# Kernel tuning notes

Hardware: AMD Instinct MI355X
Metric: run time of the kernel (lower is better)

## Reference

```python
import jax, jax.numpy as jnp
import numpy as np

N0, N1, N2 = 100000, 20000, 4000
DEG = 10
G_NODES = 200000
D, ED, CD, FF, NHEAD = 512, 256, 300, 2048, 2


def _layernorm(x, g, b, eps=1e-5):
    m = jnp.mean(x, -1, keepdims=True)
    v = jnp.var(x, -1, keepdims=True)
    return (x - m) * jax.lax.rsqrt(v + eps) * g + b


def _mha(q_in, kv_in, w_in, b_in, w_out, b_out):
    # torch nn.MultiheadAttention, inputs are (seq, batch, d)
    d = q_in.shape[-1]
    wq, wk, wv = w_in[:d], w_in[d:2 * d], w_in[2 * d:]
    bq, bk, bv = b_in[:d], b_in[d:2 * d], b_in[2 * d:]
    dh = d // NHEAD
    q = (q_in @ wq.T + bq).reshape(q_in.shape[0], q_in.shape[1], NHEAD, dh)
    k = (kv_in @ wk.T + bk).reshape(kv_in.shape[0], kv_in.shape[1], NHEAD, dh)
    v = (kv_in @ wv.T + bv).reshape(kv_in.shape[0], kv_in.shape[1], NHEAD, dh)
    scores = jnp.einsum('qnhd,knhd->nhqk', q, k) * (dh ** -0.5)
    o = jnp.einsum('nhqk,knhd->qnhd', jax.nn.softmax(scores, -1), v)
    o = o.reshape(q_in.shape[0], q_in.shape[1], d)
    return o @ w_out.T + b_out


def setup_inputs() -> dict:
    key = jax.random.key(0)
    k = lambda i: jax.random.fold_in(key, i)
    inp = {}
    inp['nid0'] = jax.random.randint(k(0), (N0,), 0, G_NODES, dtype=jnp.int32)
    inp['nid1'] = jax.random.randint(k(1), (N1,), 0, G_NODES, dtype=jnp.int32)
    inp['nid2'] = jax.random.randint(k(2), (N2,), 0, G_NODES, dtype=jnp.int32)
    inp['esrc0'] = jax.random.randint(k(3), (N1 * DEG,), 0, N0, dtype=jnp.int32)
    inp['edst0'] = jnp.repeat(jnp.arange(N1, dtype=jnp.int32), DEG)
    inp['esrc1'] = jax.random.randint(k(4), (N2 * DEG,), 0, N1, dtype=jnp.int32)
    inp['edst1'] = jnp.repeat(jnp.arange(N2, dtype=jnp.int32), DEG)
    inp['content0'] = jax.random.normal(k(5), (N0, CD), jnp.float32)
    inp['content1'] = jax.random.normal(k(6), (N1, CD), jnp.float32)
    inp['content2'] = jax.random.normal(k(7), (N2, CD), jnp.float32)
    inp['node_emb_w'] = jax.random.normal(k(8), (G_NODES + 1, ED), jnp.float32) / ED
    inp['ee_w'] = jax.random.normal(k(9), (D, ED), jnp.float32) * 0.06
    inp['ee_b'] = jax.random.normal(k(10), (D,), jnp.float32) * 0.001
    inp['proj_w'] = jax.random.normal(k(11), (D, CD), jnp.float32) * 0.06
    inp['proj_b'] = jax.random.normal(k(12), (D,), jnp.float32) * 0.001
    inp['proj_g'] = jnp.ones((D,), jnp.float32)
    inp['proj_beta'] = jnp.zeros((D,), jnp.float32)
    L = 2  # decoder layers
    inp['sa_in_w'] = jax.random.normal(k(13), (L, 3 * D, D), jnp.float32) * 0.04
    inp['sa_in_b'] = jnp.zeros((L, 3 * D), jnp.float32)
    inp['sa_out_w'] = jax.random.normal(k(14), (L, D, D), jnp.float32) * 0.04
    inp['sa_out_b'] = jnp.zeros((L, D), jnp.float32)
    inp['ca_in_w'] = jax.random.normal(k(15), (L, 3 * D, D), jnp.float32) * 0.04
    inp['ca_in_b'] = jnp.zeros((L, 3 * D), jnp.float32)
    inp['ca_out_w'] = jax.random.normal(k(16), (L, D, D), jnp.float32) * 0.04
    inp['ca_out_b'] = jnp.zeros((L, D), jnp.float32)
    inp['lin1_w'] = jax.random.normal(k(17), (L, FF, D), jnp.float32) * 0.03
    inp['lin1_b'] = jnp.zeros((L, FF), jnp.float32)
    inp['lin2_w'] = jax.random.normal(k(18), (L, D, FF), jnp.float32) * 0.03
    inp['lin2_b'] = jnp.zeros((L, D), jnp.float32)
    for n in ('n1', 'n2', 'n3'):
        inp[n + '_g'] = jnp.ones((L, D), jnp.float32)
        inp[n + '_b'] = jnp.zeros((L, D), jnp.float32)
    return inp


def _forward(nid0, nid1, nid2, esrc0, edst0, esrc1, edst1,
             content0, content1, content2, node_emb_w, ee_w, ee_b,
             proj_w, proj_b, proj_g, proj_beta,
             sa_in_w, sa_in_b, sa_out_w, sa_out_b,
             ca_in_w, ca_in_b, ca_out_w, ca_out_b,
             lin1_w, lin1_b, lin2_w, lin2_b,
             n1_g, n1_b, n2_g, n2_b, n3_g, n3_b):
    def node_h(nid, content):
        nh = node_emb_w[nid + 1] @ ee_w.T + ee_b           # emb_expand(node_emb(nid+1))
        c = _layernorm(jax.nn.leaky_relu(content @ proj_w.T + proj_b, 0.1), proj_g, proj_beta)
        h = nh + c                                          # mix_embeddings (c[:, :D] == c)
        return h / jnp.maximum(jnp.linalg.norm(h, axis=1, keepdims=True), 1e-5)

    h0 = node_h(nid0, content0)
    h1 = node_h(nid1, content1)
    h2 = node_h(nid2, content2)

    def agg_mean(h_src, src, dst, n_dst):
        s = jax.ops.segment_sum(h_src[src], dst, num_segments=n_dst)
        w = jax.ops.segment_sum(jnp.ones(src.shape[0], h_src.dtype), dst, num_segments=n_dst)
        return s / w[:, None]

    # block 0: non-prediction GraphConv -> concat(mean_agg, h), L2 normalize
    m1 = agg_mean(h0, esrc0, edst0, N1)
    h1 = jnp.concatenate([m1, h1], axis=1)                  # (N1, 2D)
    h1 = h1 / jnp.maximum(jnp.linalg.norm(h1, axis=1, keepdims=True), 1e-5)

    # block 1: prediction GraphConv -> transformer-decoder fusion
    m2 = agg_mean(h1, esrc1, edst1, N2)                     # (N2, 2D)
    mem = m2.reshape(N2, 2, D).transpose(1, 0, 2)           # (n_layer=2, N2, D)
    tgt = h2[None]                                          # (1, N2, D)
    for l in range(2):  # post-norm TransformerDecoderLayer, gelu, dropout=0
        t2 = _mha(tgt, tgt, sa_in_w[l], sa_in_b[l], sa_out_w[l], sa_out_b[l])
        tgt = _layernorm(tgt + t2, n1_g[l], n1_b[l])
        t2 = _mha(tgt, mem, ca_in_w[l], ca_in_b[l], ca_out_w[l], ca_out_b[l])
        tgt = _layernorm(tgt + t2, n2_g[l], n2_b[l])
        ff = jax.nn.gelu(tgt @ lin1_w[l].T + lin1_b[l], approximate=False) @ lin2_w[l].T + lin2_b[l]
        tgt = _layernorm(tgt + ff, n3_g[l], n3_b[l])
    out = tgt[0]                                            # squeeze -> (N2, D)
    return out / jnp.maximum(jnp.linalg.norm(out, axis=1, keepdims=True), 1e-5)


def reference(nid0, nid1, nid2, esrc0, edst0, esrc1, edst1,
              content0, content1, content2, node_emb_w, ee_w, ee_b,
              proj_w, proj_b, proj_g, proj_beta,
              sa_in_w, sa_in_b, sa_out_w, sa_out_b,
              ca_in_w, ca_in_b, ca_out_w, ca_out_b,
              lin1_w, lin1_b, lin2_w, lin2_b,
              n1_g, n1_b, n2_g, n2_b, n3_g, n3_b):
    return _forward(nid0, nid1, nid2, esrc0, edst0, esrc1, edst1,
                    content0, content1, content2, node_emb_w, ee_w, ee_b,
                    proj_w, proj_b, proj_g, proj_beta,
                    sa_in_w, sa_in_b, sa_out_w, sa_out_b,
                    ca_in_w, ca_in_b, ca_out_w, ca_out_b,
                    lin1_w, lin1_b, lin2_w, lin2_b,
                    n1_g, n1_b, n2_g, n2_b, n3_g, n3_b)
```

## Files before the change

### kernel.cpp

```cpp
#include <hip/hip_runtime.h>
#include <math.h>

static constexpr int kN0  = 100000;
static constexpr int kN1  = 20000;
static constexpr int kN2  = 4000;
static constexpr int kDeg = 10;
static constexpr int kD   = 512;
static constexpr int kFF  = 2048;
static constexpr int kRows  = 48;
static constexpr int kRowsN = 32;
static constexpr int kLdA  = 584;
static constexpr int kLdG  = 520;

using short8  = __attribute__((ext_vector_type(8))) short;
using floatx4 = __attribute__((ext_vector_type(4))) float;

__device__ inline unsigned short f2bf(float f) {
    union { float f; unsigned u; } v; v.f = f;
    unsigned r = v.u + 0x7FFFu + ((v.u >> 16) & 1u);
    return (unsigned short)(r >> 16);
}

__global__ __launch_bounds__(256) void pack_node_w_kernel(
    const float* __restrict__ ee_w, const float* __restrict__ proj_w,
    ushort* __restrict__ Bp)
{
    int tid  = blockIdx.x * 256 + threadIdx.x;
    int lane = tid & 63;
    int tile = tid >> 6;
    int n     = (tile & 31) * 16 + (lane & 15);
    int kbase = (tile >> 5) * 32 + (lane >> 4) * 8;
    ushort v[8];
    #pragma unroll
    for (int j = 0; j < 8; ++j) {
        int k = kbase + j;
        float f = 0.f;
        if (k < 256)      f = ee_w[(size_t)n * 256 + k];
        else if (k < 556) f = proj_w[(size_t)n * 300 + (k - 256)];
        v[j] = f2bf(f);
    }
    uint4 u;
    u.x = (unsigned)v[0] | ((unsigned)v[1] << 16);
    u.y = (unsigned)v[2] | ((unsigned)v[3] << 16);
    u.z = (unsigned)v[4] | ((unsigned)v[5] << 16);
    u.w = (unsigned)v[6] | ((unsigned)v[7] << 16);
    *(uint4*)(Bp + (size_t)tid * 8) = u;
}

__global__ __launch_bounds__(256) void pack512_many_kernel(
    const float* __restrict__ sa_in_w, const float* __restrict__ sa_out_w,
    const float* __restrict__ ca_in_w, const float* __restrict__ ca_out_w,
    ushort* __restrict__ dst)
{
    int y = blockIdx.y, l = y / 6, m = y % 6;
    const float* W;
    switch (m) {
        case 0: W = sa_in_w  + (size_t)l * 3 * kD * kD + (size_t)2 * kD * kD; break;
        case 1: W = sa_out_w + (size_t)l * kD * kD; break;
        case 2: W = ca_in_w  + (size_t)l * 3 * kD * kD; break;
        case 3: W = ca_in_w  + (size_t)l * 3 * kD * kD + (size_t)kD * kD; break;
        case 4: W = ca_in_w  + (size_t)l * 3 * kD * kD + (size_t)2 * kD * kD; break;
        default:W = ca_out_w + (size_t)l * kD * kD; break;
    }
    int tid  = blockIdx.x * 256 + threadIdx.x;
    int lane = tid & 63;
    int tile = tid >> 6;
    int n  = (tile & 31) * 16 + (lane & 15);
    int kb = (tile >> 5) * 32 + (lane >> 4) * 8;
    const float* src = W + (size_t)n * 512 + kb;
    ushort v[8];
    #pragma unroll
    for (int j = 0; j < 8; ++j) v[j] = f2bf(src[j]);
    uint4 u;
    u.x = (unsigned)v[0] | ((unsigned)v[1] << 16);
    u.y = (unsigned)v[2] | ((unsigned)v[3] << 16);
    u.z = (unsigned)v[4] | ((unsigned)v[5] << 16);
    u.w = (unsigned)v[6] | ((unsigned)v[7] << 16);
    *(uint4*)(dst + (size_t)y * 262144 + (size_t)tid * 8) = u;
}

__global__ __launch_bounds__(256) void pack_generic_kernel(
    const float* __restrict__ src, size_t srcStride,
    ushort* __restrict__ dst, size_t dstStride, int N, int K)
{
    int tid  = blockIdx.x * 256 + threadIdx.x;
    int NT = N >> 4;
    int lane = tid & 63;
    int tile = tid >> 6;
    int ct = tile % NT, kc = tile / NT;
    int n  = ct * 16 + (lane & 15);
    int kb = kc * 32 + (lane >> 4) * 8;
    const float* W = src + blockIdx.y * srcStride + (size_t)n * K + kb;
    ushort v[8];
    #pragma unroll
    for (int j = 0; j < 8; ++j) v[j] = f2bf(W[j]);
    uint4 u;
    u.x = (unsigned)v[0] | ((unsigned)v[1] << 16);
    u.y = (unsigned)v[2] | ((unsigned)v[3] << 16);
    u.z = (unsigned)v[4] | ((unsigned)v[5] << 16);
    u.w = (unsigned)v[6] | ((unsigned)v[7] << 16);
    *(uint4*)(dst + blockIdx.y * dstStride + (size_t)tid * 8) = u;
}

__global__ __launch_bounds__(512, 4) void node_h_mfma(
    const int* __restrict__ nid,
    const float* __restrict__ content,
    const float* __restrict__ node_emb_w,
    const ushort* __restrict__ Bp,
    const float* __restrict__ ee_b, const float* __restrict__ proj_b,
    const float* __restrict__ proj_g, const float* __restrict__ proj_beta,
    float* __restrict__ hout, int ldh, int n)
{
    __shared__ __align__(16) ushort As[kRowsN * kLdA];
    __shared__ float redS[8][kRowsN], redQ[8][kRowsN];
    __shared__ float meanv[kRowsN], rstdv[kRowsN], rowinv[kRowsN];

    const int t    = threadIdx.x;
    const int lane = t & 63;
    const int wv   = t >> 6;
    const int quad = lane >> 4;
    const int l15  = lane & 15;
    const int row0 = blockIdx.x * kRowsN;

    #pragma unroll
    for (int it = 0; it < 9; ++it) {
        int flat = it * 512 + t;
        int r  = flat / 144;
        int k4 = flat - r * 144;
        int row = row0 + r; if (row >= n) row = n - 1;
        float4 f = make_float4(0.f, 0.f, 0.f, 0.f);
        if (k4 < 64)
            f = *(const float4*)(node_emb_w + ((size_t)(nid[row] + 1)) * 256 + k4 * 4);
        else if (k4 < 139)
            f = *(const float4*)(content + (size_t)row * 300 + (k4 - 64) * 4);
        ushort4 o = make_ushort4(f2bf(f.x), f2bf(f.y), f2bf(f.z), f2bf(f.w));
        *(ushort4*)(As + (size_t)r * kLdA + k4 * 4) = o;
    }
    __syncthreads();

    floatx4 acc[2][4] = {};
    const short8* BpV = (const short8*)Bp;

    #pragma unroll
    for (int kc = 8; kc < 18; ++kc) {
        const short8* bp = BpV + (size_t)(kc * 32 + wv * 4) * 64 + lane;
        short8 b0 = bp[0], b1 = bp[64], b2 = bp[128], b3 = bp[192];
        short8 a[2];
        #pragma unroll
        for (int rt = 0; rt < 2; ++rt)
            a[rt] = *(const short8*)(As + (size_t)(rt * 16 + l15) * kLdA + kc * 32 + quad * 8);
        #pragma unroll
        for (int rt = 0; rt < 2; ++rt) {
            acc[rt][0] = __builtin_amdgcn_mfma_f32_16x16x32_bf16(a[rt], b0, acc[rt][0], 0, 0, 0);
            acc[rt][1] = __builtin_amdgcn_mfma_f32_16x16x32_bf16(a[rt], b1, acc[rt][1], 0, 0, 0);
            acc[rt][2] = __builtin_amdgcn_mfma_f32_16x16x32_bf16(a[rt], b2, acc[rt][2], 0, 0, 0);
            acc[rt][3] = __builtin_amdgcn_mfma_f32_16x16x32_bf16(a[rt], b3, acc[rt][3], 0, 0, 0);
        }
    }

    const int colbase = wv * 64 + l15;
    float pb[4], pg[4], pbt[4], eb[4];
    #pragma unroll
    for (int ct = 0; ct < 4; ++ct) {
        int c = colbase + ct * 16;
        pb[ct]  = proj_b[c];
        pg[ct]  = proj_g[c];
        pbt[ct] = proj_beta[c];
        eb[ct]  = ee_b[c];
    }

    float s8[8], q8[8];
    #pragma unroll
    for (int rt = 0; rt < 2; ++rt) {
        #pragma unroll
        for (int i = 0; i < 4; ++i) {
            float s = 0.f, q = 0.f;
            #pragma unroll
            for (int ct = 0; ct < 4; ++ct) {
                float c = acc[rt][ct][i] + pb[ct];
                c = (c >= 0.f) ? c : 0.1f * c;
                acc[rt][ct][i] = c;
                s += c; q = fmaf(c, c, q);
            }
            s8[rt * 4 + i] = s; q8[rt * 4 + i] = q;
        }
    }
    #pragma unroll
    for (int idx = 0; idx < 8; ++idx) {
        #pragma unroll
        for (int m = 1; m < 16; m <<= 1) {
            s8[idx] += __shfl_xor(s8[idx], m);
            q8[idx] += __shfl_xor(q8[idx], m);
        }
    }
    if (l15 == 0) {
        #pragma unroll
        for (int rt = 0; rt < 2; ++rt)
            #pragma unroll
            for (int i = 0; i < 4; ++i) {
                int rl = rt * 16 + quad * 4 + i;
                redS[wv][rl] = s8[rt * 4 + i];
                redQ[wv][rl] = q8[rt * 4 + i];
            }
    }
    __syncthreads();
    if (t < kRowsN) {
        float s = 0.f, q = 0.f;
        #pragma unroll
        for (int w = 0; w < 8; ++w) { s += redS[w][t]; q += redQ[w][t]; }
        float m   = s * (1.f / 512.f);
        float var = q * (1.f / 512.f) - m * m;
        meanv[t] = m;
        rstdv[t] = rsqrtf(var + 1e-5f);
    }
    __syncthreads();

    #pragma unroll
    for (int rt = 0; rt < 2; ++rt) {
        #pragma unroll
        for (int i = 0; i < 4; ++i) {
            int rl = rt * 16 + quad * 4 + i;
            float m = meanv[rl], rs = rstdv[rl];
            #pragma unroll
            for (int ct = 0; ct < 4; ++ct)
                acc[rt][ct][i] = (acc[rt][ct][i] - m) * rs * pg[ct] + pbt[ct] + eb[ct];
        }
    }

    #pragma unroll
    for (int kc = 0; kc < 8; ++kc) {
        const short8* bp = BpV + (size_t)(kc * 32 + wv * 4) * 64 + lane;
        short8 b0 = bp[0], b1 = bp[64], b2 = bp[128], b3 = bp[192];
        short8 a[2];
        #pragma unroll
        for (int rt = 0; rt < 2; ++rt)
            a[rt] = *(const short8*)(As + (size_t)(rt * 16 + l15) * kLdA + kc * 32 + quad * 8);
        #pragma unroll
        for (int rt = 0; rt < 2; ++rt) {
            acc[rt][0] = __builtin_amdgcn_mfma_f32_16x16x32_bf16(a[rt], b0, acc[rt][0], 0, 0, 0);
            acc[rt][1] = __builtin_amdgcn_mfma_f32_16x16x32_bf16(a[rt], b1, acc[rt][1], 0, 0, 0);
            acc[rt][2] = __builtin_amdgcn_mfma_f32_16x16x32_bf16(a[rt], b2, acc[rt][2], 0, 0, 0);
            acc[rt][3] = __builtin_amdgcn_mfma_f32_16x16x32_bf16(a[rt], b3, acc[rt][3], 0, 0, 0);
        }
    }

    #pragma unroll
    for (int rt = 0; rt < 2; ++rt) {
        #pragma unroll
        for (int i = 0; i < 4; ++i) {
            float psq = 0.f;
            #pragma unroll
            for (int ct = 0; ct < 4; ++ct)
                psq = fmaf(acc[rt][ct][i], acc[rt][ct][i], psq);
            q8[rt * 4 + i] = psq;
        }
    }
    #pragma unroll
    for (int idx = 0; idx < 8; ++idx)
        #pragma unroll
        for (int m = 1; m < 16; m <<= 1)
            q8[idx] += __shfl_xor(q8[idx], m);
    if (l15 == 0) {
        #pragma unroll
        for (int rt = 0; rt < 2; ++rt)
            #pragma unroll
            for (int i = 0; i < 4; ++i)
                redS[wv][rt * 16 + quad * 4 + i] = q8[rt * 4 + i];
    }
    __syncthreads();
    if (t < kRowsN) {
        float s = 0.f;
        #pragma unroll
        for (int w = 0; w < 8; ++w) s += redS[w][t];
        rowinv[t] = 1.f / fmaxf(sqrtf(s), 1e-5f);
    }
    __syncthreads();

    #pragma unroll
    for (int rt = 0; rt < 2; ++rt) {
        #pragma unroll
        for (int i = 0; i < 4; ++i) {
            int rl = rt * 16 + quad * 4 + i;
            int grow = row0 + rl;
            if (grow < n) {
                float inv = rowinv[rl];
                float* dst = hout + (size_t)grow * ldh + colbase;
                #pragma unroll
                for (int ct = 0; ct < 4; ++ct)
                    dst[ct * 16] = acc[rt][ct][i] * inv;
            }
        }
    }
}

__device__ inline float gelu_exact(float x) {
    return 0.5f * x * (1.f + erff(x * 0.70710678118654752f));
}

template<int EPI>
__global__ __launch_bounds__(512, 2) void gemm_mfma(
    const float* __restrict__ A, int lda,
    const ushort* __restrict__ Bp, const float* __restrict__ bias,
    float* __restrict__ C, int ldc,
    const float* __restrict__ resid,
    const float* __restrict__ lng, const float* __restrict__ lnb,
    int M, int K, int N)
{
    __shared__ __align__(16) ushort As[kRows * kLdG];
    __shared__ float redS[8][kRows], redQ[8][kRows];
    __shared__ float meanv[kRows], rstdv[kRows];

    const int t    = threadIdx.x;
    const int lane = t & 63;
    const int wv   = t >> 6;
    const int quad = lane >> 4;
    const int l15  = lane & 15;
    const int row0 = blockIdx.x * kRows;
    const int nb   = blockIdx.y;
    const int NT   = N >> 4;

    floatx4 acc[3][4] = {};
    const short8* BpV = (const short8*)Bp;

    for (int k0 = 0; k0 < K; k0 += 512) {
        #pragma unroll
        for (int it = 0; it < 12; ++it) {
            int flat = it * 512 + t;
            int r  = flat >> 7;
            int k4 = flat & 127;
            int row = row0 + r; if (row >= M) row = M - 1;
            float4 f = *(const float4*)(A + (size_t)row * lda + k0 + k4 * 4);
            ushort4 o = make_ushort4(f2bf(f.x), f2bf(f.y), f2bf(f.z), f2bf(f.w));
            *(ushort4*)(As + (size_t)r * kLdG + k4 * 4) = o;
        }
        __syncthreads();
        const int g0 = k0 >> 5;
        #pragma unroll
        for (int kc = 0; kc < 16; ++kc) {
            const short8* bp = BpV + ((size_t)(g0 + kc) * NT + nb * 32 + wv * 4) * 64 + lane;
            short8 b0 = bp[0], b1 = bp[64], b2 = bp[128], b3 = bp[192];
            short8 a[3];
            #pragma unroll
            for (int rt = 0; rt < 3; ++rt)
                a[rt] = *(const short8*)(As + (size_t)(rt * 16 + l15) * kLdG + kc * 32 + quad * 8);
            #pragma unroll
            for (int rt = 0; rt < 3; ++rt) {
                acc[rt][0] = __builtin_amdgcn_mfma_f32_16x16x32_bf16(a[rt], b0, acc[rt][0], 0, 0, 0);
                acc[rt][1] = __builtin_amdgcn_mfma_f32_16x16x32_bf16(a[rt], b1, acc[rt][1], 0, 0, 0);
                acc[rt][2] = __builtin_amdgcn_mfma_f32_16x16x32_bf16(a[rt], b2, acc[rt][2], 0, 0, 0);
                acc[rt][3] = __builtin_amdgcn_mfma_f32_16x16x32_bf16(a[rt], b3, acc[rt][3], 0, 0, 0);
            }
        }
        __syncthreads();
    }

    const int colloc = wv * 64 + l15;
    float b[4];
    #pragma unroll
    for (int ct = 0; ct < 4; ++ct) b[ct] = bias[nb * 512 + colloc + ct * 16];

    if constexpr (EPI == 0 || EPI == 1) {
        #pragma unroll
        for (int rt = 0; rt < 3; ++rt) {
            #pragma unroll
            for (int i = 0; i < 4; ++i) {
                int row = row0 + rt * 16 + quad * 4 + i;
                if (row < M) {
                    float* dst = C + (size_t)row * ldc + nb * 512 + colloc;
                    #pragma unroll
                    for (int ct = 0; ct < 4; ++ct) {
                        float v = acc[rt][ct][i] + b[ct];
                        if (EPI == 1) v = gelu_exact(v);
                        dst[ct * 16] = v;
                    }
                }
            }
        }
    } else {
        float lg[4], lb[4];
        #pragma unroll
        for (int ct = 0; ct < 4; ++ct) {
            lg[ct] = lng[colloc + ct * 16];
            lb[ct] = lnb[colloc + ct * 16];
        }
        float s12[12], q12[12];
        #pragma unroll
        for (int rt = 0; rt < 3; ++rt) {
            #pragma unroll
            for (int i = 0; i < 4; ++i) {
                int rl = rt * 16 + quad * 4 + i;
                int row = row0 + rl; if (row >= M) row = M - 1;
                const float* rr = resid + (size_t)row * 512 + colloc;
                float s = 0.f, q = 0.f;
                #pragma unroll
                for (int ct = 0; ct < 4; ++ct) {
                    float h = acc[rt][ct][i] + b[ct] + rr[ct * 16];
                    acc[rt][ct][i] = h;
                    s += h; q = fmaf(h, h, q);
                }
                s12[rt * 4 + i] = s; q12[rt * 4 + i] = q;
            }
        }
        #pragma unroll
        for (int idx = 0; idx < 12; ++idx) {
            #pragma unroll
            for (int m = 1; m < 16; m <<= 1) {
                s12[idx] += __shfl_xor(s12[idx], m);
                q12[idx] += __shfl_xor(q12[idx], m);
            }
        }
        if (l15 == 0) {
            #pragma unroll
            for (int rt = 0; rt < 3; ++rt)
                #pragma unroll
                for (int i = 0; i < 4; ++i) {
                    int rl = rt * 16 + quad * 4 + i;
                    redS[wv][rl] = s12[rt * 4 + i];
                    redQ[wv][rl] = q12[rt * 4 + i];
                }
        }
        __syncthreads();
        if (t < kRows) {
            float s = 0.f, q = 0.f;
            #pragma unroll
            for (int w = 0; w < 8; ++w) { s += redS[w][t]; q += redQ[w][t]; }
            float m   = s * (1.f / 512.f);
            float var = q * (1.f / 512.f) - m * m;
            meanv[t] = m;
            rstdv[t] = rsqrtf(var + 1e-5f);
        }
        __syncthreads();
        #pragma unroll
        for (int rt = 0; rt < 3; ++rt) {
            #pragma unroll
            for (int i = 0; i < 4; ++i) {
                int rl = rt * 16 + quad * 4 + i;
                int row = row0 + rl;
                if (row < M) {
                    float m = meanv[rl], rs = rstdv[rl];
                    float* dst = C + (size_t)row * 512 + colloc;
                    #pragma unroll
                    for (int ct = 0; ct < 4; ++ct)
                        dst[ct * 16] = (acc[rt][ct][i] - m) * rs * lg[ct] + lb[ct];
                }
            }
        }
    }
}

__device__ inline float block_sum256(float v, float* red4) {
    #pragma unroll
    for (int off = 32; off > 0; off >>= 1) v += __shfl_down(v, off);
    if ((threadIdx.x & 63) == 0) red4[threadIdx.x >> 6] = v;
    __syncthreads();
    return red4[0] + red4[1] + red4[2] + red4[3];
}

__global__ __launch_bounds__(256) void agg_norm1_kernel(
    const float* __restrict__ h0, const int* __restrict__ esrc,
    float* __restrict__ h1cat)
{
    __shared__ int idx[kDeg];
    __shared__ float red4[4];
    int i = blockIdx.x, t = threadIdx.x;
    if (t < kDeg) idx[t] = esrc[i * kDeg + t];
    __syncthreads();
    float s0 = 0.f, s1 = 0.f;
    for (int e = 0; e < kDeg; ++e) {
        const float* hr = h0 + (size_t)idx[e] * 512;
        s0 += hr[t]; s1 += hr[t + 256];
    }
    s0 *= 0.1f; s1 *= 0.1f;
    size_t base = (size_t)i * 1024;
    float o0 = h1cat[base + 512 + t];
    float o1 = h1cat[base + 768 + t];
    float tot = block_sum256(s0 * s0 + s1 * s1 + o0 * o0 + o1 * o1, red4);
    float inv = 1.f / fmaxf(sqrtf(tot), 1e-5f);
    h1cat[base + t]       = s0 * inv;
    h1cat[base + 256 + t] = s1 * inv;
    h1cat[base + 512 + t] = o0 * inv;
    h1cat[base + 768 + t] = o1 * inv;
}

__global__ __launch_bounds__(256) void agg2_kernel(
    const float* __restrict__ h1cat, const int* __restrict__ esrc,
    float* __restrict__ m2)
{
    __shared__ int idx[kDeg];
    int i = blockIdx.x, t = threadIdx.x;
    if (t < kDeg) idx[t] = esrc[i * kDeg + t];
    __syncthreads();
    float s0 = 0.f, s1 = 0.f, s2 = 0.f, s3 = 0.f;
    for (int e = 0; e < kDeg; ++e) {
        const float* hr = h1cat + (size_t)idx[e] * 1024;
        s0 += hr[t]; s1 += hr[t + 256]; s2 += hr[t + 512]; s3 += hr[t + 768];
    }
    size_t base = (size_t)i * 1024;
    m2[base + t]       = s0 * 0.1f;
    m2[base + 256 + t] = s1 * 0.1f;
    m2[base + 512 + t] = s2 * 0.1f;
    m2[base + 768 + t] = s3 * 0.1f;
}

__global__ __launch_bounds__(256) void attn_combine_kernel(
    const float* __restrict__ Q,
    const float* __restrict__ Kb, const float* __restrict__ Vb,
    float* __restrict__ O)
{
    __shared__ float red[4][4];
    __shared__ float a[4];
    int i = blockIdx.x, t = threadIdx.x;
    size_t base  = (size_t)i * 512;
    size_t base0 = (size_t)(2 * i) * 512;
    size_t base1 = base0 + 512;
    float q0 = Q[base + t], q1 = Q[base + t + 256];
    float p00 = q0 * Kb[base0 + t];
    float p01 = q0 * Kb[base1 + t];
    float p10 = q1 * Kb[base0 + t + 256];
    float p11 = q1 * Kb[base1 + t + 256];
    #pragma unroll
    for (int off = 32; off > 0; off >>= 1) {
        p00 += __shfl_down(p00, off);
        p01 += __shfl_down(p01, off);
        p10 += __shfl_down(p10, off);
        p11 += __shfl_down(p11, off);
    }
    int w = t >> 6;
    if ((t & 63) == 0) { red[w][0] = p00; red[w][1] = p01; red[w][2] = p10; red[w][3] = p11; }
    __syncthreads();
    if (t == 0) {
        float s00 = (red[0][0] + red[1][0] + red[2][0] + red[3][0]) * 0.0625f;
        float s01 = (red[0][1] + red[1][1] + red[2][1] + red[3][1]) * 0.0625f;
        float s10 = (red[0][2] + red[1][2] + red[2][2] + red[3][2]) * 0.0625f;
        float s11 = (red[0][3] + red[1][3] + red[2][3] + red[3][3]) * 0.0625f;
        float m0 = fmaxf(s00, s01);
        float e0 = expf(s00 - m0), e1 = expf(s01 - m0);
        float d0 = e0 + e1;
        a[0] = e0 / d0; a[1] = e1 / d0;
        float m1 = fmaxf(s10, s11);
        float f0 = expf(s10 - m1), f1 = expf(s11 - m1);
        float d1 = f0 + f1;
        a[2] = f0 / d1; a[3] = f1 / d1;
    }
    __syncthreads();
    O[base + t]       = a[0] * Vb[base0 + t]       + a[1] * Vb[base1 + t];
    O[base + t + 256] = a[2] * Vb[base0 + t + 256] + a[3] * Vb[base1 + t + 256];
}

__global__ __launch_bounds__(256) void final_norm_kernel(
    const float* __restrict__ tgt, float* __restrict__ out)
{
    __shared__ float red4[4];
    int i = blockIdx.x, t = threadIdx.x;
    size_t base = (size_t)i * 512;
    float v0 = tgt[base + t], v1 = tgt[base + t + 256];
    float tot = block_sum256(v0 * v0 + v1 * v1, red4);
    float inv = 1.f / fmaxf(sqrtf(tot), 1e-5f);
    out[base + t]       = v0 * inv;
    out[base + t + 256] = v1 * inv;
}

extern "C" void kernel_launch(void* const* d_in, const int* in_sizes, int n_in,
                              void* d_out, int out_size, void* d_ws, size_t ws_size,
                              hipStream_t stream)
{
    (void)in_sizes; (void)n_in; (void)out_size; (void)ws_size;
    const int*   nid0       = (const int*)d_in[0];
    const int*   nid1       = (const int*)d_in[1];
    const int*   nid2       = (const int*)d_in[2];
    const int*   esrc0      = (const int*)d_in[3];
    const int*   esrc1      = (const int*)d_in[5];
    const float* content0   = (const float*)d_in[7];
    const float* content1   = (const float*)d_in[8];
    const float* content2   = (const float*)d_in[9];
    const float* node_emb_w = (const float*)d_in[10];
    const float* ee_w       = (const float*)d_in[11];
    const float* ee_b       = (const float*)d_in[12];
    const float* proj_w     = (const float*)d_in[13];
    const float* proj_b     = (const float*)d_in[14];
    const float* proj_g     = (const float*)d_in[15];
    const float* proj_beta  = (const float*)d_in[16];
    const float* sa_in_w    = (const float*)d_in[17];
    const float* sa_in_b    = (const float*)d_in[18];
    const float* sa_out_w   = (const float*)d_in[19];
    const float* sa_out_b   = (const float*)d_in[20];
    const float* ca_in_w    = (const float*)d_in[21];
    const float* ca_in_b    = (const float*)d_in[22];
    const float* ca_out_w   = (const float*)d_in[23];
    const float* ca_out_b   = (const float*)d_in[24];
    const float* lin1_w     = (const float*)d_in[25];
    const float* lin1_b     = (const float*)d_in[26];
    const float* lin2_w     = (const float*)d_in[27];
    const float* lin2_b     = (const float*)d_in[28];
    const float* n1_g       = (const float*)d_in[29];
    const float* n1_b       = (const float*)d_in[30];
    const float* n2_g       = (const float*)d_in[31];
    const float* n2_b       = (const float*)d_in[32];
    const float* n3_g       = (const float*)d_in[33];
    const float* n3_b       = (const float*)d_in[34];

    float* ws = (float*)d_ws;
    size_t off = 0;
    float* h0    = ws + off; off += (size_t)kN0 * 512;
    float* h1cat = ws + off; off += (size_t)kN1 * 1024;
    float* m2    = ws + off; off += (size_t)kN2 * 1024;
    float* tgt   = ws + off; off += (size_t)kN2 * 512;
    float* Qb    = ws + off; off += (size_t)kN2 * 512;
    float* Kb    = ws + off; off += (size_t)2 * kN2 * 512;
    float* Vb    = ws + off; off += (size_t)2 * kN2 * 512;
    float* Ob    = ws + off; off += (size_t)kN2 * 512;
    float* ffh   = ws + off; off += (size_t)kN2 * 2048;
    ushort* BpNode = (ushort*)(ws + off); off += 147456;
    ushort* Pw512  = (ushort*)(ws + off); off += 12 * 262144 / 2;
    ushort* Pl1    = (ushort*)(ws + off); off += 2 * 1048576 / 2;
    ushort* Pl2    = (ushort*)(ws + off); off += 2 * 1048576 / 2;

    dim3 blk(256);

    pack_node_w_kernel<<<dim3(144), blk, 0, stream>>>(ee_w, proj_w, BpNode);
    pack512_many_kernel<<<dim3(128, 12), blk, 0, stream>>>(
        sa_in_w, sa_out_w, ca_in_w, ca_out_w, Pw512);
    pack_generic_kernel<<<dim3(512, 2), blk, 0, stream>>>(
        lin1_w, (size_t)kFF * kD, Pl1, 1048576, kFF, kD);
    pack_generic_kernel<<<dim3(512, 2), blk, 0, stream>>>(
        lin2_w, (size_t)kD * kFF, Pl2, 1048576, kD, kFF);

    node_h_mfma<<<dim3((kN0 + kRowsN - 1) / kRowsN), dim3(512), 0, stream>>>(
        nid0, content0, node_emb_w, BpNode, ee_b, proj_b, proj_g, proj_beta,
        h0, 512, kN0);
    node_h_mfma<<<dim3((kN1 + kRowsN - 1) / kRowsN), dim3(512), 0, stream>>>(
        nid1, content1, node_emb_w, BpNode, ee_b, proj_b, proj_g, proj_beta,
        h1cat + 512, 1024, kN1);
    node_h_mfma<<<dim3((kN2 + kRowsN - 1) / kRowsN), dim3(512), 0, stream>>>(
        nid2, content2, node_emb_w, BpNode, ee_b, proj_b, proj_g, proj_beta,
        tgt, 512, kN2);

    agg_norm1_kernel<<<dim3(kN1), blk, 0, stream>>>(h0, esrc0, h1cat);
    agg2_kernel<<<dim3(kN2), blk, 0, stream>>>(h1cat, esrc1, m2);

    const int M   = kN2;
    const int gM  = (M + kRows - 1) / kRows;
    const int gM2 = (2 * M + kRows - 1) / kRows;
    dim3 blk512(512);
    for (int l = 0; l < 2; ++l) {
        const ushort* sa_v_p   = Pw512 + (size_t)(l * 6 + 0) * 262144;
        const ushort* sa_out_p = Pw512 + (size_t)(l * 6 + 1) * 262144;
        const ushort* ca_q_p   = Pw512 + (size_t)(l * 6 + 2) * 262144;
        const ushort* ca_k_p   = Pw512 + (size_t)(l * 6 + 3) * 262144;
        const ushort* ca_v_p   = Pw512 + (size_t)(l * 6 + 4) * 262144;
        const ushort* ca_out_p = Pw512 + (size_t)(l * 6 + 5) * 262144;
        const ushort* l1_p     = Pl1 + (size_t)l * 1048576;
        const ushort* l2_p     = Pl2 + (size_t)l * 1048576;
        const float* sa_b = sa_in_b + (size_t)l * 3 * kD;
        const float* saob = sa_out_b + (size_t)l * kD;
        const float* ca_b = ca_in_b + (size_t)l * 3 * kD;
        const float* caob = ca_out_b + (size_t)l * kD;
        const float* l1b = lin1_b + (size_t)l * kFF;
        const float* l2b = lin2_b + (size_t)l * kD;

        gemm_mfma<0><<<dim3(gM, 1), blk512, 0, stream>>>(
            tgt, 512, sa_v_p, sa_b + 2 * kD, Qb, 512,
            nullptr, nullptr, nullptr, M, 512, 512);
        gemm_mfma<2><<<dim3(gM, 1), blk512, 0, stream>>>(
            Qb, 512, sa_out_p, saob, tgt, 512,
            tgt, n1_g + l * kD, n1_b + l * kD, M, 512, 512);

        gemm_mfma<0><<<dim3(gM, 1), blk512, 0, stream>>>(
            tgt, 512, ca_q_p, ca_b, Qb, 512,
            nullptr, nullptr, nullptr, M, 512, 512);
        gemm_mfma<0><<<dim3(gM2, 1), blk512, 0, stream>>>(
            m2, 512, ca_k_p, ca_b + kD, Kb, 512,
            nullptr, nullptr, nullptr, 2 * M, 512, 512);
        gemm_mfma<0><<<dim3(gM2, 1), blk512, 0, stream>>>(
            m2, 512, ca_v_p, ca_b + 2 * kD, Vb, 512,
            nullptr, nullptr, nullptr, 2 * M, 512, 512);
        attn_combine_kernel<<<dim3(M), blk, 0, stream>>>(Qb, Kb, Vb, Ob);
        gemm_mfma<2><<<dim3(gM, 1), blk512, 0, stream>>>(
            Ob, 512, ca_out_p, caob, tgt, 512,
            tgt, n2_g + l * kD, n2_b + l * kD, M, 512, 512);

        gemm_mfma<1><<<dim3(gM, 4), blk512, 0, stream>>>(
            tgt, 512, l1_p, l1b, ffh, 2048,
            nullptr, nullptr, nullptr, M, 512, 2048);
        gemm_mfma<2><<<dim3(gM, 1), blk512, 0, stream>>>(
            ffh, 2048, l2_p, l2b, tgt, 512,
            tgt, n3_g + l * kD, n3_b + l * kD, M, 2048, 512);
    }

    final_norm_kernel<<<dim3(kN2), blk, 0, stream>>>(tgt, (float*)d_out);
}
```

Before: 1.165 ms.

## Retile node projection to 64 rows and shrink transformer GEMM tiles to 16 rows

The node embedding/projection kernel now handles 64 rows per block instead of 32, so each packed weight fragment read from global memory is reused across four row tiles. Node ids are cached in shared memory so each row's id is loaded once rather than per element. The transformer GEMM drops from 48-row to 16-row tiles with a higher occupancy launch bound, giving more blocks for the small M=4000 problem at the cost of less weight reuse per block. The larger node tile raises register and LDS use (about 75KB LDS), which may limit occupancy.

```diff
diff --git a/kernel.cpp b/kernel.cpp
--- a/kernel.cpp
+++ b/kernel.cpp
@@ -7,8 +7,8 @@
 static constexpr int kDeg = 10;
 static constexpr int kD   = 512;
 static constexpr int kFF  = 2048;
-static constexpr int kRows  = 48;
-static constexpr int kRowsN = 32;
+static constexpr int kRowsG = 16;
+static constexpr int kRowsN = 64;
 static constexpr int kLdA  = 584;
 static constexpr int kLdG  = 520;
 
@@ -112,6 +112,7 @@
     float* __restrict__ hout, int ldh, int n)
 {
     __shared__ __align__(16) ushort As[kRowsN * kLdA];
+    __shared__ int nids[kRowsN];
     __shared__ float redS[8][kRowsN], redQ[8][kRowsN];
     __shared__ float meanv[kRowsN], rstdv[kRowsN], rowinv[kRowsN];
 
@@ -122,35 +123,42 @@
     const int l15  = lane & 15;
     const int row0 = blockIdx.x * kRowsN;
 
-    #pragma unroll
-    for (int it = 0; it < 9; ++it) {
+    if (t < kRowsN) {
+        int row = row0 + t; if (row >= n) row = n - 1;
+        nids[t] = nid[row] + 1;
+    }
+    __syncthreads();
+
+    #pragma unroll
+    for (int it = 0; it < 18; ++it) {
         int flat = it * 512 + t;
         int r  = flat / 144;
         int k4 = flat - r * 144;
-        int row = row0 + r; if (row >= n) row = n - 1;
         float4 f = make_float4(0.f, 0.f, 0.f, 0.f);
         if (k4 < 64)
-            f = *(const float4*)(node_emb_w + ((size_t)(nid[row] + 1)) * 256 + k4 * 4);
-        else if (k4 < 139)
+            f = *(const float4*)(node_emb_w + (size_t)nids[r] * 256 + k4 * 4);
+        else if (k4 < 139) {
+            int row = row0 + r; if (row >= n) row = n - 1;
             f = *(const float4*)(content + (size_t)row * 300 + (k4 - 64) * 4);
+        }
         ushort4 o = make_ushort4(f2bf(f.x), f2bf(f.y), f2bf(f.z), f2bf(f.w));
         *(ushort4*)(As + (size_t)r * kLdA + k4 * 4) = o;
     }
     __syncthreads();
 
-    floatx4 acc[2][4] = {};
+    floatx4 acc[4][4] = {};
     const short8* BpV = (const short8*)Bp;
 
     #pragma unroll
     for (int kc = 8; kc < 18; ++kc) {
         const short8* bp = BpV + (size_t)(kc * 32 + wv * 4) * 64 + lane;
         short8 b0 = bp[0], b1 = bp[64], b2 = bp[128], b3 = bp[192];
-        short8 a[2];
-        #pragma unroll
-        for (int rt = 0; rt < 2; ++rt)
+        short8 a[4];
+        #pragma unroll
+        for (int rt = 0; rt < 4; ++rt)
             a[rt] = *(const short8*)(As + (size_t)(rt * 16 + l15) * kLdA + kc * 32 + quad * 8);
         #pragma unroll
-        for (int rt = 0; rt < 2; ++rt) {
+        for (int rt = 0; rt < 4; ++rt) {
             acc[rt][0] = __builtin_amdgcn_mfma_f32_16x16x32_bf16(a[rt], b0, acc[rt][0], 0, 0, 0);
             acc[rt][1] = __builtin_amdgcn_mfma_f32_16x16x32_bf16(a[rt], b1, acc[rt][1], 0, 0, 0);
             acc[rt][2] = __builtin_amdgcn_mfma_f32_16x16x32_bf16(a[rt], b2, acc[rt][2], 0, 0, 0);
@@ -169,9 +177,9 @@
         eb[ct]  = ee_b[c];
     }
 
-    float s8[8], q8[8];
-    #pragma unroll
-    for (int rt = 0; rt < 2; ++rt) {
+    float s16[16], q16[16];
+    #pragma unroll
+    for (int rt = 0; rt < 4; ++rt) {
         #pragma unroll
         for (int i = 0; i < 4; ++i) {
             float s = 0.f, q = 0.f;
@@ -182,25 +190,25 @@
                 acc[rt][ct][i] = c;
                 s += c; q = fmaf(c, c, q);
             }
-            s8[rt * 4 + i] = s; q8[rt * 4 + i] = q;
-        }
-    }
-    #pragma unroll
-    for (int idx = 0; idx < 8; ++idx) {
+            s16[rt * 4 + i] = s; q16[rt * 4 + i] = q;
+        }
+    }
+    #pragma unroll
+    for (int idx = 0; idx < 16; ++idx) {
         #pragma unroll
         for (int m = 1; m < 16; m <<= 1) {
-            s8[idx] += __shfl_xor(s8[idx], m);
-            q8[idx] += __shfl_xor(q8[idx], m);
+            s16[idx] += __shfl_xor(s16[idx], m);
+            q16[idx] += __shfl_xor(q16[idx], m);
         }
     }
     if (l15 == 0) {
         #pragma unroll
-        for (int rt = 0; rt < 2; ++rt)
+        for (int rt = 0; rt < 4; ++rt)
             #pragma unroll
             for (int i = 0; i < 4; ++i) {
                 int rl = rt * 16 + quad * 4 + i;
-                redS[wv][rl] = s8[rt * 4 + i];
-                redQ[wv][rl] = q8[rt * 4 + i];
+                redS[wv][rl] = s16[rt * 4 + i];
+                redQ[wv][rl] = q16[rt * 4 + i];
             }
     }
     __syncthreads();
@@ -216,7 +224,7 @@
     __syncthreads();
 
     #pragma unroll
-    for (int rt = 0; rt < 2; ++rt) {
+    for (int rt = 0; rt < 4; ++rt) {
         #pragma unroll
         for (int i = 0; i < 4; ++i) {
             int rl = rt * 16 + quad * 4 + i;
@@ -231,12 +239,12 @@
     for (int kc = 0; kc < 8; ++kc) {
         const short8* bp = BpV + (size_t)(kc * 32 + wv * 4) * 64 + lane;
         short8 b0 = bp[0], b1 = bp[64], b2 = bp[128], b3 = bp[192];
-        short8 a[2];
-        #pragma unroll
-        for (int rt = 0; rt < 2; ++rt)
+        short8 a[4];
+        #pragma unroll
+        for (int rt = 0; rt < 4; ++rt)
             a[rt] = *(const short8*)(As + (size_t)(rt * 16 + l15) * kLdA + kc * 32 + quad * 8);
         #pragma unroll
-        for (int rt = 0; rt < 2; ++rt) {
+        for (int rt = 0; rt < 4; ++rt) {
             acc[rt][0] = __builtin_amdgcn_mfma_f32_16x16x32_bf16(a[rt], b0, acc[rt][0], 0, 0, 0);
             acc[rt][1] = __builtin_amdgcn_mfma_f32_16x16x32_bf16(a[rt], b1, acc[rt][1], 0, 0, 0);
             acc[rt][2] = __builtin_amdgcn_mfma_f32_16x16x32_bf16(a[rt], b2, acc[rt][2], 0, 0, 0);
@@ -245,27 +253,27 @@
     }
 
     #pragma unroll
-    for (int rt = 0; rt < 2; ++rt) {
+    for (int rt = 0; rt < 4; ++rt) {
         #pragma unroll
         for (int i = 0; i < 4; ++i) {
             float psq = 0.f;
             #pragma unroll
             for (int ct = 0; ct < 4; ++ct)
                 psq = fmaf(acc[rt][ct][i], acc[rt][ct][i], psq);
-            q8[rt * 4 + i] = psq;
-        }
-    }
-    #pragma unroll
-    for (int idx = 0; idx < 8; ++idx)
+            q16[rt * 4 + i] = psq;
+        }
+    }
+    #pragma unroll
+    for (int idx = 0; idx < 16; ++idx)
         #pragma unroll
         for (int m = 1; m < 16; m <<= 1)
-            q8[idx] += __shfl_xor(q8[idx], m);
+            q16[idx] += __shfl_xor(q16[idx], m);
     if (l15 == 0) {
         #pragma unroll
-        for (int rt = 0; rt < 2; ++rt)
+        for (int rt = 0; rt < 4; ++rt)
             #pragma unroll
             for (int i = 0; i < 4; ++i)
-                redS[wv][rt * 16 + quad * 4 + i] = q8[rt * 4 + i];
+                redS[wv][rt * 16 + quad * 4 + i] = q16[rt * 4 + i];
     }
     __syncthreads();
     if (t < kRowsN) {
@@ -277,7 +285,7 @@
     __syncthreads();
 
     #pragma unroll
-    for (int rt = 0; rt < 2; ++rt) {
+    for (int rt = 0; rt < 4; ++rt) {
         #pragma unroll
         for (int i = 0; i < 4; ++i) {
             int rl = rt * 16 + quad * 4 + i;
@@ -298,7 +306,7 @@
 }
 
 template<int EPI>
-__global__ __launch_bounds__(512, 2) void gemm_mfma(
+__global__ __launch_bounds__(512, 4) void gemm_mfma(
     const float* __restrict__ A, int lda,
     const ushort* __restrict__ Bp, const float* __restrict__ bias,
     float* __restrict__ C, int ldc,
@@ -306,25 +314,25 @@
     const float* __restrict__ lng, const float* __restrict__ lnb,
     int M, int K, int N)
 {
-    __shared__ __align__(16) ushort As[kRows * kLdG];
-    __shared__ float redS[8][kRows], redQ[8][kRows];
-    __shared__ float meanv[kRows], rstdv[kRows];
+    __shared__ __align__(16) ushort As[kRowsG * kLdG];
+    __shared__ float redS[8][kRowsG], redQ[8][kRowsG];
+    __shared__ float meanv[kRowsG], rstdv[kRowsG];
 
     const int t    = threadIdx.x;
     const int lane = t & 63;
     const int wv   = t >> 6;
     const int quad = lane >> 4;
     const int l15  = lane & 15;
-    const int row0 = blockIdx.x * kRows;
+    const int row0 = blockIdx.x * kRowsG;
     const int nb   = blockIdx.y;
     const int NT   = N >> 4;
 
-    floatx4 acc[3][4] = {};
+    floatx4 acc[4] = {};
     const short8* BpV = (const short8*)Bp;
 
     for (int k0 = 0; k0 < K; k0 += 512) {
         #pragma unroll
-        for (int it = 0; it < 12; ++it) {
+        for (int it = 0; it < 4; ++it) {
             int flat = it * 512 + t;
             int r  = flat >> 7;
             int k4 = flat & 127;
@@ -339,17 +347,11 @@
         for (int kc = 0; kc < 16; ++kc) {
             const short8* bp = BpV + ((size_t)(g0 + kc) * NT + nb * 32 + wv * 4) * 64 + lane;
             short8 b0 = bp[0], b1 = bp[64], b2 = bp[128], b3 = bp[192];
-            short8 a[3];
-            #pragma unroll
-            for (int rt = 0; rt < 3; ++rt)
-                a[rt] = *(const short8*)(As + (size_t)(rt * 16 + l15) * kLdG + kc * 32 + quad * 8);
-            #pragma unroll
-            for (int rt = 0; rt < 3; ++rt) {
-                acc[rt][0] = __builtin_amdgcn_mfma_f32_16x16x32_bf16(a[rt], b0, acc[rt][0], 0, 0, 0);
-                acc[rt][1] = __builtin_amdgcn_mfma_f32_16x16x32_bf16(a[rt], b1, acc[rt][1], 0, 0, 0);
-                acc[rt][2] = __builtin_amdgcn_mfma_f32_16x16x32_bf16(a[rt], b2, acc[rt][2], 0, 0, 0);
-                acc[rt][3] = __builtin_amdgcn_mfma_f32_16x16x32_bf16(a[rt], b3, acc[rt][3], 0, 0, 0);
-            }
+            short8 a = *(const short8*)(As + (size_t)l15 * kLdG + kc * 32 + quad * 8);
+            acc[0] = __builtin_amdgcn_mfma_f32_16x16x32_bf16(a, b0, acc[0], 0, 0, 0);
+            acc[1] = __builtin_amdgcn_mfma_f32_16x16x32_bf16(a, b1, acc[1], 0, 0, 0);
+            acc[2] = __builtin_amdgcn_mfma_f32_16x16x32_bf16(a, b2, acc[2], 0, 0, 0);
+            acc[3] = __builtin_amdgcn_mfma_f32_16x16x32_bf16(a, b3, acc[3], 0, 0, 0);
         }
         __syncthreads();
     }
@@ -361,18 +363,15 @@
 
     if constexpr (EPI == 0 || EPI == 1) {
         #pragma unroll
-        for (int rt = 0; rt < 3; ++rt) {
-            #pragma unroll
-            for (int i = 0; i < 4; ++i) {
-                int row = row0 + rt * 16 + quad * 4 + i;
-                if (row < M) {
-                    float* dst = C + (size_t)row * ldc + nb * 512 + colloc;
-                    #pragma unroll
-                    for (int ct = 0; ct < 4; ++ct) {
-                        float v = acc[rt][ct][i] + b[ct];
-                        if (EPI == 1) v = gelu_exact(v);
-                        dst[ct * 16] = v;
-                    }
+        for (int i = 0; i < 4; ++i) {
+            int row = row0 + quad * 4 + i;
+            if (row < M) {
+                float* dst = C + (size_t)row * ldc + nb * 512 + colloc;
+                #pragma unroll
+                for (int ct = 0; ct < 4; ++ct) {
+                    float v = acc[ct][i] + b[ct];
+                    if (EPI == 1) v = gelu_exact(v);
+                    dst[ct * 16] = v;
                 }
             }
         }
@@ -383,44 +382,39 @@
             lg[ct] = lng[colloc + ct * 16];
             lb[ct] = lnb[colloc + ct * 16];
         }
-        float s12[12], q12[12];
-        #pragma unroll
-        for (int rt = 0; rt < 3; ++rt) {
+        float s4[4], q4[4];
+        #pragma unroll
+        for (int i = 0; i < 4; ++i) {
+            int rl = quad * 4 + i;
+            int row = row0 + rl; if (row >= M) row = M - 1;
+            const float* rr = resid + (size_t)row * 512 + colloc;
+            float s = 0.f, q = 0.f;
+            #pragma unroll
+            for (int ct = 0; ct < 4; ++ct) {
+                float h = acc[ct][i] + b[ct] + rr[ct * 16];
+                acc[ct][i] = h;
+                s += h; q = fmaf(h, h, q);
+            }
+            s4[i] = s; q4[i] = q;
+        }
+        #pragma unroll
+        for (int idx = 0; idx < 4; ++idx) {
+            #pragma unroll
+            for (int m = 1; m < 16; m <<= 1) {
+                s4[idx] += __shfl_xor(s4[idx], m);
+                q4[idx] += __shfl_xor(q4[idx], m);
+            }
+        }
+        if (l15 == 0) {
             #pragma unroll
             for (int i = 0; i < 4; ++i) {
-                int rl = rt * 16 + quad * 4 + i;
-                int row = row0 + rl; if (row >= M) row = M - 1;
-                const float* rr = resid + (size_t)row * 512 + colloc;
-                float s = 0.f, q = 0.f;
-                #pragma unroll
-                for (int ct = 0; ct < 4; ++ct) {
-                    float h = acc[rt][ct][i] + b[ct] + rr[ct * 16];
-                    acc[rt][ct][i] = h;
-                    s += h; q = fmaf(h, h, q);
-                }
-                s12[rt * 4 + i] = s; q12[rt * 4 + i] = q;
-            }
-        }
-        #pragma unroll
-        for (int idx = 0; idx < 12; ++idx) {
-            #pragma unroll
-            for (int m = 1; m < 16; m <<= 1) {
-                s12[idx] += __shfl_xor(s12[idx], m);
-                q12[idx] += __shfl_xor(q12[idx], m);
-            }
-        }
-        if (l15 == 0) {
-            #pragma unroll
-            for (int rt = 0; rt < 3; ++rt)
-                #pragma unroll
-                for (int i = 0; i < 4; ++i) {
-                    int rl = rt * 16 + quad * 4 + i;
-                    redS[wv][rl] = s12[rt * 4 + i];
-                    redQ[wv][rl] = q12[rt * 4 + i];
-                }
+                int rl = quad * 4 + i;
+                redS[wv][rl] = s4[i];
+                redQ[wv][rl] = q4[i];
+            }
         }
         __syncthreads();
-        if (t < kRows) {
+        if (t < kRowsG) {
             float s = 0.f, q = 0.f;
             #pragma unroll
             for (int w = 0; w < 8; ++w) { s += redS[w][t]; q += redQ[w][t]; }
@@ -431,18 +425,15 @@
         }
         __syncthreads();
         #pragma unroll
-        for (int rt = 0; rt < 3; ++rt) {
-            #pragma unroll
-            for (int i = 0; i < 4; ++i) {
-                int rl = rt * 16 + quad * 4 + i;
-                int row = row0 + rl;
-                if (row < M) {
-                    float m = meanv[rl], rs = rstdv[rl];
-                    float* dst = C + (size_t)row * 512 + colloc;
-                    #pragma unroll
-                    for (int ct = 0; ct < 4; ++ct)
-                        dst[ct * 16] = (acc[rt][ct][i] - m) * rs * lg[ct] + lb[ct];
-                }
+        for (int i = 0; i < 4; ++i) {
+            int rl = quad * 4 + i;
+            int row = row0 + rl;
+            if (row < M) {
+                float m = meanv[rl], rs = rstdv[rl];
+                float* dst = C + (size_t)row * 512 + colloc;
+                #pragma unroll
+                for (int ct = 0; ct < 4; ++ct)
+                    dst[ct * 16] = (acc[ct][i] - m) * rs * lg[ct] + lb[ct];
             }
         }
     }
@@ -639,8 +630,8 @@
     agg2_kernel<<<dim3(kN2), blk, 0, stream>>>(h1cat, esrc1, m2);
 
     const int M   = kN2;
-    const int gM  = (M + kRows - 1) / kRows;
-    const int gM2 = (2 * M + kRows - 1) / kRows;
+    const int gM  = (M + kRowsG - 1) / kRowsG;
+    const int gM2 = (2 * M + kRowsG - 1) / kRowsG;
     dim3 blk512(512);
     for (int l = 0; l < 2; ++l) {
         const ushort* sa_v_p   = Pw512 + (size_t)(l * 6 + 0) * 262144;
```

After: 1.287 ms. 10.4% more time.
